# Performance work log

Hardware: AMD Instinct MI355X
Metric: run time of the kernel (lower is better)

The kernel has to match this reference:

```python
import jax, jax.numpy as jnp
import numpy as np
from jax import lax

B, S, D, H, O = 128, 256, 128, 512, 25
TEMP = 0.1


def _init(key, shape, scale):
    return jax.random.uniform(key, shape, jnp.float32, -scale, scale)


def setup_inputs() -> dict:
    key = jax.random.key(0)
    ks = jax.random.split(key, 24)
    sH = 1.0 / np.sqrt(H)
    s2H = 1.0 / np.sqrt(2 * H)
    sD = 1.0 / np.sqrt(D)
    inp = {
        "x": jax.random.normal(ks[0], (B, S, D), jnp.float32),
        "noise_u": jnp.clip(jax.random.uniform(ks[1], (S, B, 1), jnp.float32), 1e-6, 1 - 1e-6),
        # layer_cin: Linear(D, H)
        "w_cin": _init(ks[2], (D, H), sD), "b_cin": _init(ks[3], (H,), sD),
        # layer_c MLP: 2H->2H (x3, ReLU) -> 1
        "w1": _init(ks[4], (2 * H, 2 * H), s2H), "b1": _init(ks[5], (2 * H,), s2H),
        "w2": _init(ks[6], (2 * H, 2 * H), s2H), "b2": _init(ks[7], (2 * H,), s2H),
        "w3": _init(ks[8], (2 * H, 2 * H), s2H), "b3": _init(ks[9], (2 * H,), s2H),
        "w4": _init(ks[10], (2 * H, 1), s2H), "b4": _init(ks[11], (1,), s2H),
        # GRUCell(H, H): gates ordered (r, z, n)
        "w_ih": _init(ks[12], (H, 3 * H), sH), "b_ih": _init(ks[13], (3 * H,), sH),
        "w_hh": _init(ks[14], (H, 3 * H), sH), "b_hh": _init(ks[15], (3 * H,), sH),
        # output Linear(H, O)
        "w_out": _init(ks[16], (H, O), sH), "b_out": _init(ks[17], (O,), sH),
    }
    return inp


def _gru_cell(x, h, w_ih, b_ih, w_hh, b_hh):
    gx = x @ w_ih + b_ih  # [B, 3H]
    gh = h @ w_hh + b_hh
    xr, xz, xn = jnp.split(gx, 3, axis=-1)
    hr, hz, hn = jnp.split(gh, 3, axis=-1)
    r = jax.nn.sigmoid(xr + hr)
    z = jax.nn.sigmoid(xz + hz)
    n = jnp.tanh(xn + r * hn)
    return (1.0 - z) * n + z * h


def reference(x, noise_u, w_cin, b_cin, w1, b1, w2, b2, w3, b3, w4, b4,
              w_ih, b_ih, w_hh, b_hh, w_out, b_out):
    xs = jnp.transpose(x, (1, 0, 2))  # [S, B, D]

    def step(carry, inp):
        c, h, n = carry
        x_t, u = inp
        c_in = jnp.tanh(x_t @ w_cin + b_cin)  # [B, H]
        com = jnp.concatenate([c, c_in], axis=1)  # [B, 2H]
        z = jax.nn.relu(com @ w1 + b1)
        z = jax.nn.relu(z @ w2 + b2)
        z = jax.nn.relu(z @ w3 + b3)
        alpha_logit = z @ w4 + b4  # [B, 1]
        # RelaxedBernoulli(temp=0.1).sample(): sigmoid((logits + logistic noise)/T), detached
        logistic = jnp.log(u) - jnp.log1p(-u)
        alpha = lax.stop_gradient(jax.nn.sigmoid((alpha_logit + logistic) / TEMP))
        h_gru = _gru_cell(c, h, w_ih, b_ih, w_hh, b_hh)
        h_new = h * (1.0 - alpha) + alpha * h_gru
        new_n = n * (1.0 - alpha) + 1.0
        c_new = (c * n * (1.0 - alpha) + c_in) / new_n
        return (c_new, h_new, new_n), None

    c0 = jnp.zeros((B, H), x.dtype)
    h0 = jnp.zeros((B, H), x.dtype)
    n0 = jnp.zeros((B, 1), x.dtype)
    (c, h, n), _ = lax.scan(step, (c0, h0, n0), (xs, noise_u))
    h = _gru_cell(c, h, w_ih, b_ih, w_hh, b_hh)  # final post-loop GRU step
    return h @ w_out + b_out
```

## Files before the change

kernel.cpp:

```cpp
#include <hip/hip_runtime.h>
#include <math.h>

#define SLEN 256
#define BSZ  128
#define DIN  128
#define HSZ  512
#define HH2  1024
#define GG3  1536
#define OSZ  25

typedef _Float16 h8 __attribute__((ext_vector_type(8)));
typedef float    f4 __attribute__((ext_vector_type(4)));

struct P_t {
  const float *x, *noise, *b_cin, *b1, *b2, *b3, *w4, *b4, *b_ih, *b_hh, *w_out, *b_out;
  _Float16 *WT1, *WT2, *WT3, *WTih, *WThh, *WTcin;
  _Float16 *FW1, *FW2, *FW3, *FWih, *FWhh;
  _Float16 *CIN, *COMlo, *Z1, *Z2, *HF16;
  float *LOGI, *GX, *GH, *PART, *HF32, *CF32, *NF32;
  float *out;
};

__device__ __forceinline__ f4 mfma16(h8 a, h8 b, f4 c) {
  return __builtin_amdgcn_mfma_f32_16x16x32_f16(a, b, c, 0, 0, 0);
}

__global__ __launch_bounds__(256) void transpose_cvt(const float* __restrict__ src,
    _Float16* __restrict__ dst, int K, int N) {
  __shared__ float tl[32][33];
  int nt = N >> 5;
  int bx = blockIdx.x % nt, by = blockIdx.x / nt;
  int n0 = bx << 5, k0 = by << 5;
  int tx = threadIdx.x & 31, ty = threadIdx.x >> 5;
#pragma unroll
  for (int i = 0; i < 4; ++i) {
    int r = ty + (i << 3);
    tl[r][tx] = src[(size_t)(k0 + r) * N + n0 + tx];
  }
  __syncthreads();
#pragma unroll
  for (int i = 0; i < 4; ++i) {
    int r = ty + (i << 3);
    dst[(size_t)(n0 + r) * K + k0 + tx] = (_Float16)tl[tx][r];
  }
}

__global__ __launch_bounds__(512) void fragpack(const _Float16* __restrict__ src,
    _Float16* __restrict__ dst, int K) {
  int ct = blockIdx.x;
  int chunks = (K / 32) * 64;
  for (int idx = threadIdx.x; idx < chunks; idx += 512) {
    int i = idx >> 6, lane = idx & 63;
    int mlw = lane & 15, qw = lane >> 4;
    *(h8*)(dst + ((size_t)ct * (K / 32) + i) * 512 + (size_t)lane * 8) =
        *(const h8*)(src + ((size_t)ct * 16 + mlw) * K + i * 32 + qw * 8);
  }
}

__global__ __launch_bounds__(256) void cin_kernel(P_t P) {
  int tid = blockIdx.x * blockDim.x + threadIdx.x;
  if (tid < SLEN * BSZ) {
    float u = P.noise[tid];
    P.LOGI[tid] = logf(u) - log1pf(-u);
  }
  int gw = tid >> 6, lane = tid & 63;
  int nw = (gridDim.x * blockDim.x) >> 6;
  int ml = lane & 15, q = lane >> 4;
  const int MT = (SLEN * BSZ) / 16;
  for (int tt = gw; tt < MT * 8; tt += nw) {
    int mt = tt & (MT - 1), nt = tt / MT;
    int m0 = mt * 16, n0 = nt * 64;
    int m = m0 + ml, b = m & 127, s = m >> 7;
    const float* ap = P.x + ((size_t)b * SLEN + s) * DIN + q * 8;
    const _Float16* bp = P.WTcin + (size_t)(n0 + ml) * DIN + q * 8;
    f4 a0 = {0,0,0,0}, a1 = a0, a2 = a0, a3 = a0;
#pragma unroll
    for (int k = 0; k < DIN; k += 32) {
      f4 lo = *(const f4*)(ap + k);
      f4 hi = *(const f4*)(ap + k + 4);
      h8 av;
      av[0] = (_Float16)lo[0]; av[1] = (_Float16)lo[1];
      av[2] = (_Float16)lo[2]; av[3] = (_Float16)lo[3];
      av[4] = (_Float16)hi[0]; av[5] = (_Float16)hi[1];
      av[6] = (_Float16)hi[2]; av[7] = (_Float16)hi[3];
      a0 = mfma16(av, *(const h8*)(bp + k),            a0);
      a1 = mfma16(av, *(const h8*)(bp + 16*DIN + k),   a1);
      a2 = mfma16(av, *(const h8*)(bp + 32*DIN + k),   a2);
      a3 = mfma16(av, *(const h8*)(bp + 48*DIN + k),   a3);
    }
#pragma unroll
    for (int r = 0; r < 4; ++r) {
      int row = m0 + q * 4 + r;
      int c0 = n0 + ml;
      P.CIN[(size_t)row * HSZ + c0     ] = (_Float16)tanhf(a0[r] + P.b_cin[c0]);
      P.CIN[(size_t)row * HSZ + c0 + 16] = (_Float16)tanhf(a1[r] + P.b_cin[c0 + 16]);
      P.CIN[(size_t)row * HSZ + c0 + 32] = (_Float16)tanhf(a2[r] + P.b_cin[c0 + 32]);
      P.CIN[(size_t)row * HSZ + c0 + 48] = (_Float16)tanhf(a3[r] + P.b_cin[c0 + 48]);
    }
  }
}

__global__ __launch_bounds__(256) void init_kernel(P_t P) {
  int idx = blockIdx.x * 256 + threadIdx.x;
  if (idx < BSZ * HSZ) {
    P.HF32[idx] = 0.f; P.CF32[idx] = 0.f;
    P.HF16[idx] = (_Float16)0.f; P.COMlo[idx] = (_Float16)0.f;
  }
  if (idx < BSZ) P.NF32[idx] = 0.f;
}

__global__ __launch_bounds__(256) void step_a(P_t P, int t, int base) {
  const int tid = threadIdx.x;
  const int lane = tid & 63, wv = tid >> 6;
  const int ml = lane & 15, q = lane >> 4;
  const int g = base + blockIdx.x * 4 + wv;
  f4 acc = {0.f, 0.f, 0.f, 0.f};
  if (g < 512) {
    int rt = g & 7, ct = g >> 3;
    int m0 = rt * 16, col = ct * 16 + ml;
    const _Float16* a0 = P.COMlo + (size_t)(m0 + ml) * HSZ + q * 8;
    const _Float16* a1 = P.CIN + ((size_t)t * BSZ + m0 + ml) * HSZ + q * 8;
    const _Float16* bp = P.FW1 + (size_t)ct * 32 * 512 + (size_t)lane * 8;
#pragma unroll
    for (int i = 0; i < 16; ++i)
      acc = mfma16(*(const h8*)(a0 + i * 32), *(const h8*)(bp + (size_t)i * 512), acc);
#pragma unroll
    for (int i = 0; i < 16; ++i)
      acc = mfma16(*(const h8*)(a1 + i * 32), *(const h8*)(bp + (size_t)(16 + i) * 512), acc);
    float bia = P.b1[col];
#pragma unroll
    for (int j = 0; j < 4; ++j)
      P.Z1[(size_t)(m0 + q * 4 + j) * HH2 + col] = (_Float16)fmaxf(acc[j] + bia, 0.f);
  } else if (g < 1280) {
    int u = g - 512, rt = u & 7, ct = u >> 3;
    int m0 = rt * 16, col = ct * 16 + ml;
    const _Float16* a0 = P.COMlo + (size_t)(m0 + ml) * HSZ + q * 8;
    const _Float16* bp = P.FWih + (size_t)ct * 16 * 512 + (size_t)lane * 8;
#pragma unroll
    for (int i = 0; i < 16; ++i)
      acc = mfma16(*(const h8*)(a0 + i * 32), *(const h8*)(bp + (size_t)i * 512), acc);
    float bia = P.b_ih[col];
#pragma unroll
    for (int j = 0; j < 4; ++j)
      P.GX[(size_t)(m0 + q * 4 + j) * GG3 + col] = acc[j] + bia;
  } else {
    int u = g - 1280, rt = u & 7, ct = u >> 3;
    int m0 = rt * 16, col = ct * 16 + ml;
    const _Float16* a0 = P.HF16 + (size_t)(m0 + ml) * HSZ + q * 8;
    const _Float16* bp = P.FWhh + (size_t)ct * 16 * 512 + (size_t)lane * 8;
#pragma unroll
    for (int i = 0; i < 16; ++i)
      acc = mfma16(*(const h8*)(a0 + i * 32), *(const h8*)(bp + (size_t)i * 512), acc);
    float bia = P.b_hh[col];
#pragma unroll
    for (int j = 0; j < 4; ++j)
      P.GH[(size_t)(m0 + q * 4 + j) * GG3 + col] = acc[j] + bia;
  }
}

__global__ __launch_bounds__(256) void step_b(P_t P) {
  const int tid = threadIdx.x;
  const int lane = tid & 63, wv = tid >> 6;
  const int ml = lane & 15, q = lane >> 4;
  const int g = blockIdx.x * 4 + wv;
  int rt = g & 7, ct = g >> 3;
  int m0 = rt * 16, col = ct * 16 + ml;
  const _Float16* a0 = P.Z1 + (size_t)(m0 + ml) * HH2 + q * 8;
  const _Float16* bp = P.FW2 + (size_t)ct * 32 * 512 + (size_t)lane * 8;
  f4 acc = {0.f, 0.f, 0.f, 0.f};
#pragma unroll
  for (int i = 0; i < 32; ++i)
    acc = mfma16(*(const h8*)(a0 + i * 32), *(const h8*)(bp + (size_t)i * 512), acc);
  float bia = P.b2[col];
#pragma unroll
  for (int j = 0; j < 4; ++j)
    P.Z2[(size_t)(m0 + q * 4 + j) * HH2 + col] = (_Float16)fmaxf(acc[j] + bia, 0.f);
}

__global__ __launch_bounds__(256) void step_c(P_t P) {
  const int tid = threadIdx.x;
  const int lane = tid & 63, wv = tid >> 6;
  const int ml = lane & 15, q = lane >> 4;
  const int g = blockIdx.x * 4 + wv;
  int rt = g & 7, ct = g >> 3;
  int m0 = rt * 16, col = ct * 16 + ml;
  const _Float16* a0 = P.Z2 + (size_t)(m0 + ml) * HH2 + q * 8;
  const _Float16* bp = P.FW3 + (size_t)ct * 32 * 512 + (size_t)lane * 8;
  f4 acc = {0.f, 0.f, 0.f, 0.f};
#pragma unroll
  for (int i = 0; i < 32; ++i)
    acc = mfma16(*(const h8*)(a0 + i * 32), *(const h8*)(bp + (size_t)i * 512), acc);
  float bia = P.b3[col], w4v = P.w4[col];
#pragma unroll
  for (int j = 0; j < 4; ++j) {
    float v = fmaxf(acc[j] + bia, 0.f) * w4v;
    v += __shfl_xor(v, 1); v += __shfl_xor(v, 2);
    v += __shfl_xor(v, 4); v += __shfl_xor(v, 8);
    if (ml == 0) P.PART[(size_t)ct * BSZ + m0 + q * 4 + j] = v;
  }
}

__global__ __launch_bounds__(512) void step_d(P_t P, int t) {
  __shared__ float sa[4];
  const int r = blockIdx.x, tid = threadIdx.x;
  if (tid < 64) {
    float v = P.PART[(size_t)tid * BSZ + r];
#pragma unroll
    for (int off = 32; off > 0; off >>= 1) v += __shfl_xor(v, off);
    if (tid == 0) {
      float lg = (v + P.b4[0] + P.LOGI[(size_t)t * BSZ + r]) * 10.0f;
      float alpha = 1.f / (1.f + expf(-lg));
      float om = 1.f - alpha;
      float n_old = P.NF32[r];
      float nnew = n_old * om + 1.f;
      P.NF32[r] = nnew;
      sa[0] = alpha; sa[1] = om; sa[2] = n_old * om; sa[3] = nnew;
    }
  }
  __syncthreads();
  float alpha = sa[0], om = sa[1], nom = sa[2], nnew = sa[3];
  int col = tid;
  size_t go = (size_t)r * GG3 + col;
  float xr = P.GX[go], xz = P.GX[go + 512], xn = P.GX[go + 1024];
  float hr = P.GH[go], hz = P.GH[go + 512], hn = P.GH[go + 1024];
  float rg = 1.f / (1.f + expf(-(xr + hr)));
  float zg = 1.f / (1.f + expf(-(xz + hz)));
  float ng = tanhf(xn + rg * hn);
  size_t ho = (size_t)r * HSZ + col;
  float h_old = P.HF32[ho];
  float hg = (1.f - zg) * ng + zg * h_old;
  float hnew = h_old * om + alpha * hg;
  P.HF32[ho] = hnew; P.HF16[ho] = (_Float16)hnew;
  float c_old = P.CF32[ho];
  float cin_t = (float)P.CIN[((size_t)t * BSZ + r) * HSZ + col];
  float cnew = (c_old * nom + cin_t) / nnew;
  P.CF32[ho] = cnew; P.COMlo[ho] = (_Float16)cnew;
}

__global__ __launch_bounds__(512) void final_kernel(P_t P) {
  __shared__ float hf[512];
  const int r = blockIdx.x, tid = threadIdx.x;
  const int lane = tid & 63, wv = tid >> 6;
  {
    int col = tid;
    size_t go = (size_t)r * GG3 + col;
    float xr = P.GX[go], xz = P.GX[go + 512], xn = P.GX[go + 1024];
    float hr = P.GH[go], hz = P.GH[go + 512], hn = P.GH[go + 1024];
    float rg = 1.f / (1.f + expf(-(xr + hr)));
    float zg = 1.f / (1.f + expf(-(xz + hz)));
    float ng = tanhf(xn + rg * hn);
    float h_old = P.HF32[(size_t)r * HSZ + col];
    hf[col] = (1.f - zg) * ng + zg * h_old;
  }
  __syncthreads();
  for (int c = wv; c < OSZ; c += 8) {
    float v = 0.f;
#pragma unroll
    for (int j = 0; j < 8; ++j)
      v += hf[lane + 64 * j] * P.w_out[(size_t)(lane + 64 * j) * OSZ + c];
#pragma unroll
    for (int off = 32; off > 0; off >>= 1) v += __shfl_xor(v, off);
    if (lane == 0) P.out[r * OSZ + c] = v + P.b_out[c];
  }
}

extern "C" void kernel_launch(void* const* d_in, const int* in_sizes, int n_in,
                              void* d_out, int out_size, void* d_ws, size_t ws_size,
                              hipStream_t stream) {
  const float* x     = (const float*)d_in[0];
  const float* noise = (const float*)d_in[1];
  const float* w_cin = (const float*)d_in[2];
  const float* b_cin = (const float*)d_in[3];
  const float* w1    = (const float*)d_in[4];
  const float* b1    = (const float*)d_in[5];
  const float* w2    = (const float*)d_in[6];
  const float* b2    = (const float*)d_in[7];
  const float* w3    = (const float*)d_in[8];
  const float* b3    = (const float*)d_in[9];
  const float* w4    = (const float*)d_in[10];
  const float* b4    = (const float*)d_in[11];
  const float* w_ih  = (const float*)d_in[12];
  const float* b_ih  = (const float*)d_in[13];
  const float* w_hh  = (const float*)d_in[14];
  const float* b_hh  = (const float*)d_in[15];
  const float* w_out = (const float*)d_in[16];
  const float* b_out = (const float*)d_in[17];

  char* ws = (char*)d_ws;
  size_t off = 0;
  auto alloc = [&](size_t bytes) -> void* {
    void* p = ws + off;
    off = (off + bytes + 255) & ~(size_t)255;
    return p;
  };

  P_t P;
  P.x = x; P.noise = noise; P.b_cin = b_cin; P.b1 = b1; P.b2 = b2; P.b3 = b3;
  P.w4 = w4; P.b4 = b4; P.b_ih = b_ih; P.b_hh = b_hh; P.w_out = w_out; P.b_out = b_out;
  P.WT1   = (_Float16*)alloc((size_t)HH2 * HH2 * 2);
  P.WT2   = (_Float16*)alloc((size_t)HH2 * HH2 * 2);
  P.WT3   = (_Float16*)alloc((size_t)HH2 * HH2 * 2);
  P.WTih  = (_Float16*)alloc((size_t)GG3 * HSZ * 2);
  P.WThh  = (_Float16*)alloc((size_t)GG3 * HSZ * 2);
  P.WTcin = (_Float16*)alloc((size_t)HSZ * DIN * 2);
  P.FW1   = (_Float16*)alloc((size_t)HH2 * HH2 * 2);
  P.FW2   = (_Float16*)alloc((size_t)HH2 * HH2 * 2);
  P.FW3   = (_Float16*)alloc((size_t)HH2 * HH2 * 2);
  P.FWih  = (_Float16*)alloc((size_t)GG3 * HSZ * 2);
  P.FWhh  = (_Float16*)alloc((size_t)GG3 * HSZ * 2);
  P.CIN   = (_Float16*)alloc((size_t)SLEN * BSZ * HSZ * 2);
  P.COMlo = (_Float16*)alloc((size_t)BSZ * HSZ * 2);
  P.Z1    = (_Float16*)alloc((size_t)BSZ * HH2 * 2);
  P.Z2    = (_Float16*)alloc((size_t)BSZ * HH2 * 2);
  P.HF16  = (_Float16*)alloc((size_t)BSZ * HSZ * 2);
  P.LOGI  = (float*)alloc((size_t)SLEN * BSZ * 4);
  P.GX    = (float*)alloc((size_t)BSZ * GG3 * 4);
  P.GH    = (float*)alloc((size_t)BSZ * GG3 * 4);
  P.PART  = (float*)alloc((size_t)64 * BSZ * 4);
  P.HF32  = (float*)alloc((size_t)BSZ * HSZ * 4);
  P.CF32  = (float*)alloc((size_t)BSZ * HSZ * 4);
  P.NF32  = (float*)alloc((size_t)BSZ * 4);
  P.out   = (float*)d_out;

  transpose_cvt<<<(HH2/32)*(HH2/32), 256, 0, stream>>>(w1, P.WT1, HH2, HH2);
  transpose_cvt<<<(HH2/32)*(HH2/32), 256, 0, stream>>>(w2, P.WT2, HH2, HH2);
  transpose_cvt<<<(HH2/32)*(HH2/32), 256, 0, stream>>>(w3, P.WT3, HH2, HH2);
  transpose_cvt<<<(GG3/32)*(HSZ/32), 256, 0, stream>>>(w_ih, P.WTih, HSZ, GG3);
  transpose_cvt<<<(GG3/32)*(HSZ/32), 256, 0, stream>>>(w_hh, P.WThh, HSZ, GG3);
  transpose_cvt<<<(HSZ/32)*(DIN/32), 256, 0, stream>>>(w_cin, P.WTcin, DIN, HSZ);
  fragpack<<<HH2/16, 512, 0, stream>>>(P.WT1, P.FW1, HH2);
  fragpack<<<HH2/16, 512, 0, stream>>>(P.WT2, P.FW2, HH2);
  fragpack<<<HH2/16, 512, 0, stream>>>(P.WT3, P.FW3, HH2);
  fragpack<<<GG3/16, 512, 0, stream>>>(P.WTih, P.FWih, HSZ);
  fragpack<<<GG3/16, 512, 0, stream>>>(P.WThh, P.FWhh, HSZ);

  cin_kernel<<<1024, 256, 0, stream>>>(P);
  init_kernel<<<256, 256, 0, stream>>>(P);

  for (int t = 0; t < SLEN; ++t) {
    step_a<<<512, 256, 0, stream>>>(P, t, 0);
    step_b<<<128, 256, 0, stream>>>(P);
    step_c<<<128, 256, 0, stream>>>(P);
    step_d<<<BSZ, 512, 0, stream>>>(P, t);
  }
  step_a<<<384, 256, 0, stream>>>(P, 0, 512);
  final_kernel<<<BSZ, 512, 0, stream>>>(P);
}
```

Before: 6.966 ms.

## Fuse GRU/state update into next step's GEMM kernel with double-buffered state

This removes the separate per-timestep state-update kernel. Each step_a block now reduces the alpha partials itself, recomputes the c and h updates for its 16-row tile into shared memory as the fp16 GEMM operand, and has one designated block write the fp32 state back. h, c, n, GX and GH are double-buffered by timestep parity so reads and writes don't race, and the PART layout is transposed for vectorized reduction. The aim is to cut one kernel launch and a global round-trip per step. In exchange, GX/GH reads and the sigmoid/tanh work are done redundantly across many blocks.

```diff
diff --git a/kernel.cpp b/kernel.cpp
--- a/kernel.cpp
+++ b/kernel.cpp
@@ -16,7 +16,7 @@
   const float *x, *noise, *b_cin, *b1, *b2, *b3, *w4, *b4, *b_ih, *b_hh, *w_out, *b_out;
   _Float16 *WT1, *WT2, *WT3, *WTih, *WThh, *WTcin;
   _Float16 *FW1, *FW2, *FW3, *FWih, *FWhh;
-  _Float16 *CIN, *COMlo, *Z1, *Z2, *HF16;
+  _Float16 *CIN, *Z1, *Z2;
   float *LOGI, *GX, *GH, *PART, *HF32, *CF32, *NF32;
   float *out;
 };
@@ -24,6 +24,7 @@
 __device__ __forceinline__ f4 mfma16(h8 a, h8 b, f4 c) {
   return __builtin_amdgcn_mfma_f32_16x16x32_f16(a, b, c, 0, 0, 0);
 }
+__device__ __forceinline__ float sigmf(float x) { return 1.f / (1.f + expf(-x)); }
 
 __global__ __launch_bounds__(256) void transpose_cvt(const float* __restrict__ src,
     _Float16* __restrict__ dst, int K, int N) {
@@ -103,58 +104,135 @@
 __global__ __launch_bounds__(256) void init_kernel(P_t P) {
   int idx = blockIdx.x * 256 + threadIdx.x;
   if (idx < BSZ * HSZ) {
-    P.HF32[idx] = 0.f; P.CF32[idx] = 0.f;
-    P.HF16[idx] = (_Float16)0.f; P.COMlo[idx] = (_Float16)0.f;
-  }
-  if (idx < BSZ) P.NF32[idx] = 0.f;
-}
-
-__global__ __launch_bounds__(256) void step_a(P_t P, int t, int base) {
-  const int tid = threadIdx.x;
-  const int lane = tid & 63, wv = tid >> 6;
+    P.HF32[idx] = 0.f; P.HF32[idx + BSZ * HSZ] = 0.f;
+    P.CF32[idx] = 0.f; P.CF32[idx + BSZ * HSZ] = 0.f;
+  }
+  if (idx < 2 * BSZ) P.NF32[idx] = 0.f;
+}
+
+__global__ __launch_bounds__(256) void step_a(P_t P, int t, int tail) {
+  __shared__ __align__(16) _Float16 sA[8192];
+  __shared__ float s_al[16], s_om[16], s_nom[16], s_nnew[16];
+  const int tid = threadIdx.x, lane = tid & 63, wv = tid >> 6;
   const int ml = lane & 15, q = lane >> 4;
-  const int g = base + blockIdx.x * 4 + wv;
+  const int b = blockIdx.x + (tail ? 128 : 0);
+  int role, rt, cg;
+  if (b < 128)      { role = 0; rt = b >> 4; cg = b & 15; }
+  else if (b < 320) { int u = b - 128; role = 1; rt = u / 24; cg = u - rt * 24; }
+  else              { int u = b - 320; role = 2; rt = u / 24; cg = u - rt * 24; }
+  const int m0 = rt * 16;
+  const int pm1 = (t + 1) & 1;
+  const int pm2 = t & 1;
+
+  if (t > 0) {
+    if (wv == 0) {
+      const float* pp = P.PART + (size_t)(m0 + ml) * 64 + q * 16;
+      f4 p0 = *(const f4*)pp, p1 = *(const f4*)(pp + 4),
+         p2 = *(const f4*)(pp + 8), p3 = *(const f4*)(pp + 12);
+      float s = p0[0]+p0[1]+p0[2]+p0[3] + p1[0]+p1[1]+p1[2]+p1[3]
+              + p2[0]+p2[1]+p2[2]+p2[3] + p3[0]+p3[1]+p3[2]+p3[3];
+      s += __shfl_xor(s, 16); s += __shfl_xor(s, 32);
+      float lg = (s + P.b4[0] + P.LOGI[(size_t)(t - 1) * BSZ + m0 + ml]) * 10.0f;
+      float al = sigmf(lg), om = 1.f - al;
+      if (q == 0) {
+        float n_old = P.NF32[pm2 * BSZ + m0 + ml];
+        float nom = n_old * om, nnew = nom + 1.f;
+        s_al[ml] = al; s_om[ml] = om; s_nom[ml] = nom; s_nnew[ml] = nnew;
+        if (role == 0 && cg == 0) P.NF32[pm1 * BSZ + m0 + ml] = nnew;
+      }
+    }
+    __syncthreads();
+    if (role <= 1) {
+      float nom = s_nom[ml], rnn = 1.f / s_nnew[ml];
+      const float*    cf = P.CF32 + ((size_t)pm2 * BSZ + m0 + ml) * HSZ;
+      const _Float16* ci = P.CIN + ((size_t)(t - 1) * BSZ + m0 + ml) * HSZ;
+      float* cw = (role == 0 && cg == 0)
+                  ? (P.CF32 + ((size_t)pm1 * BSZ + m0 + ml) * HSZ) : nullptr;
+#pragma unroll
+      for (int ic = 0; ic < 4; ++ic) {
+        int i = wv * 4 + ic, colb = i * 32 + q * 8;
+        f4 c0 = *(const f4*)(cf + colb), c1 = *(const f4*)(cf + colb + 4);
+        h8 cin8 = *(const h8*)(ci + colb);
+        h8 hv; f4 o0, o1;
+#pragma unroll
+        for (int j = 0; j < 4; ++j) {
+          o0[j] = (c0[j] * nom + (float)cin8[j])     * rnn;
+          o1[j] = (c1[j] * nom + (float)cin8[4 + j]) * rnn;
+          hv[j] = (_Float16)o0[j]; hv[4 + j] = (_Float16)o1[j];
+        }
+        *(h8*)(sA + i * 512 + lane * 8) = hv;
+        if (cw) { *(f4*)(cw + colb) = o0; *(f4*)(cw + colb + 4) = o1; }
+      }
+    } else {
+      float al = s_al[ml], om = s_om[ml];
+      const float* gx = P.GX + (size_t)pm1 * BSZ * GG3 + (size_t)(m0 + ml) * GG3;
+      const float* gh = P.GH + (size_t)pm1 * BSZ * GG3 + (size_t)(m0 + ml) * GG3;
+      const float* hf = P.HF32 + ((size_t)pm2 * BSZ + m0 + ml) * HSZ;
+      float* hw = (cg == 0) ? (P.HF32 + ((size_t)pm1 * BSZ + m0 + ml) * HSZ) : nullptr;
+#pragma unroll
+      for (int ic = 0; ic < 4; ++ic) {
+        int i = wv * 4 + ic, colb = i * 32 + q * 8;
+        f4 xr0 = *(const f4*)(gx + colb),        xr1 = *(const f4*)(gx + colb + 4);
+        f4 xz0 = *(const f4*)(gx + colb + 512),  xz1 = *(const f4*)(gx + colb + 516);
+        f4 xn0 = *(const f4*)(gx + colb + 1024), xn1 = *(const f4*)(gx + colb + 1028);
+        f4 hr0 = *(const f4*)(gh + colb),        hr1 = *(const f4*)(gh + colb + 4);
+        f4 hz0 = *(const f4*)(gh + colb + 512),  hz1 = *(const f4*)(gh + colb + 516);
+        f4 hn0 = *(const f4*)(gh + colb + 1024), hn1 = *(const f4*)(gh + colb + 1028);
+        f4 h0 = *(const f4*)(hf + colb), h1 = *(const f4*)(hf + colb + 4);
+        h8 hv; f4 o0, o1;
+#pragma unroll
+        for (int j = 0; j < 4; ++j) {
+          float rg = sigmf(xr0[j] + hr0[j]);
+          float zg = sigmf(xz0[j] + hz0[j]);
+          float ng = tanhf(xn0[j] + rg * hn0[j]);
+          o0[j] = h0[j] * om + al * ((1.f - zg) * ng + zg * h0[j]);
+          rg = sigmf(xr1[j] + hr1[j]);
+          zg = sigmf(xz1[j] + hz1[j]);
+          ng = tanhf(xn1[j] + rg * hn1[j]);
+          o1[j] = h1[j] * om + al * ((1.f - zg) * ng + zg * h1[j]);
+          hv[j] = (_Float16)o0[j]; hv[4 + j] = (_Float16)o1[j];
+        }
+        *(h8*)(sA + i * 512 + lane * 8) = hv;
+        if (hw) { *(f4*)(hw + colb) = o0; *(f4*)(hw + colb + 4) = o1; }
+      }
+    }
+  } else {
+    h8 z;
+#pragma unroll
+    for (int j = 0; j < 8; ++j) z[j] = (_Float16)0.f;
+    for (int idx = tid; idx < 1024; idx += 256) *(h8*)(sA + idx * 8) = z;
+  }
+  __syncthreads();
+
+  const int ct = cg * 4 + wv;
   f4 acc = {0.f, 0.f, 0.f, 0.f};
-  if (g < 512) {
-    int rt = g & 7, ct = g >> 3;
-    int m0 = rt * 16, col = ct * 16 + ml;
-    const _Float16* a0 = P.COMlo + (size_t)(m0 + ml) * HSZ + q * 8;
-    const _Float16* a1 = P.CIN + ((size_t)t * BSZ + m0 + ml) * HSZ + q * 8;
-    const _Float16* bp = P.FW1 + (size_t)ct * 32 * 512 + (size_t)lane * 8;
+  if (role == 0) {
+    const _Float16* bp = P.FW1 + (size_t)ct * 32 * 512 + lane * 8;
+    const _Float16* sa = sA + lane * 8;
+    const _Float16* ci = P.CIN + ((size_t)t * BSZ + m0 + ml) * HSZ + q * 8;
 #pragma unroll
     for (int i = 0; i < 16; ++i)
-      acc = mfma16(*(const h8*)(a0 + i * 32), *(const h8*)(bp + (size_t)i * 512), acc);
+      acc = mfma16(*(const h8*)(sa + i * 512), *(const h8*)(bp + (size_t)i * 512), acc);
 #pragma unroll
     for (int i = 0; i < 16; ++i)
-      acc = mfma16(*(const h8*)(a1 + i * 32), *(const h8*)(bp + (size_t)(16 + i) * 512), acc);
+      acc = mfma16(*(const h8*)(ci + i * 32), *(const h8*)(bp + (size_t)(16 + i) * 512), acc);
+    int col = ct * 16 + ml;
     float bia = P.b1[col];
 #pragma unroll
     for (int j = 0; j < 4; ++j)
       P.Z1[(size_t)(m0 + q * 4 + j) * HH2 + col] = (_Float16)fmaxf(acc[j] + bia, 0.f);
-  } else if (g < 1280) {
-    int u = g - 512, rt = u & 7, ct = u >> 3;
-    int m0 = rt * 16, col = ct * 16 + ml;
-    const _Float16* a0 = P.COMlo + (size_t)(m0 + ml) * HSZ + q * 8;
-    const _Float16* bp = P.FWih + (size_t)ct * 16 * 512 + (size_t)lane * 8;
+  } else {
+    const _Float16* bp = ((role == 1) ? P.FWih : P.FWhh) + (size_t)ct * 16 * 512 + lane * 8;
+    const _Float16* sa = sA + lane * 8;
 #pragma unroll
     for (int i = 0; i < 16; ++i)
-      acc = mfma16(*(const h8*)(a0 + i * 32), *(const h8*)(bp + (size_t)i * 512), acc);
-    float bia = P.b_ih[col];
+      acc = mfma16(*(const h8*)(sa + i * 512), *(const h8*)(bp + (size_t)i * 512), acc);
+    int col = ct * 16 + ml;
+    float bia = (role == 1) ? P.b_ih[col] : P.b_hh[col];
+    float* gd = ((role == 1) ? P.GX : P.GH) + (size_t)pm2 * BSZ * GG3;
 #pragma unroll
     for (int j = 0; j < 4; ++j)
-      P.GX[(size_t)(m0 + q * 4 + j) * GG3 + col] = acc[j] + bia;
-  } else {
-    int u = g - 1280, rt = u & 7, ct = u >> 3;
-    int m0 = rt * 16, col = ct * 16 + ml;
-    const _Float16* a0 = P.HF16 + (size_t)(m0 + ml) * HSZ + q * 8;
-    const _Float16* bp = P.FWhh + (size_t)ct * 16 * 512 + (size_t)lane * 8;
-#pragma unroll
-    for (int i = 0; i < 16; ++i)
-      acc = mfma16(*(const h8*)(a0 + i * 32), *(const h8*)(bp + (size_t)i * 512), acc);
-    float bia = P.b_hh[col];
-#pragma unroll
-    for (int j = 0; j < 4; ++j)
-      P.GH[(size_t)(m0 + q * 4 + j) * GG3 + col] = acc[j] + bia;
+      gd[(size_t)(m0 + q * 4 + j) * GG3 + col] = acc[j] + bia;
   }
 }
 
@@ -196,45 +274,8 @@
     float v = fmaxf(acc[j] + bia, 0.f) * w4v;
     v += __shfl_xor(v, 1); v += __shfl_xor(v, 2);
     v += __shfl_xor(v, 4); v += __shfl_xor(v, 8);
-    if (ml == 0) P.PART[(size_t)ct * BSZ + m0 + q * 4 + j] = v;
-  }
-}
-
-__global__ __launch_bounds__(512) void step_d(P_t P, int t) {
-  __shared__ float sa[4];
-  const int r = blockIdx.x, tid = threadIdx.x;
-  if (tid < 64) {
-    float v = P.PART[(size_t)tid * BSZ + r];
-#pragma unroll
-    for (int off = 32; off > 0; off >>= 1) v += __shfl_xor(v, off);
-    if (tid == 0) {
-      float lg = (v + P.b4[0] + P.LOGI[(size_t)t * BSZ + r]) * 10.0f;
-      float alpha = 1.f / (1.f + expf(-lg));
-      float om = 1.f - alpha;
-      float n_old = P.NF32[r];
-      float nnew = n_old * om + 1.f;
-      P.NF32[r] = nnew;
-      sa[0] = alpha; sa[1] = om; sa[2] = n_old * om; sa[3] = nnew;
-    }
-  }
-  __syncthreads();
-  float alpha = sa[0], om = sa[1], nom = sa[2], nnew = sa[3];
-  int col = tid;
-  size_t go = (size_t)r * GG3 + col;
-  float xr = P.GX[go], xz = P.GX[go + 512], xn = P.GX[go + 1024];
-  float hr = P.GH[go], hz = P.GH[go + 512], hn = P.GH[go + 1024];
-  float rg = 1.f / (1.f + expf(-(xr + hr)));
-  float zg = 1.f / (1.f + expf(-(xz + hz)));
-  float ng = tanhf(xn + rg * hn);
-  size_t ho = (size_t)r * HSZ + col;
-  float h_old = P.HF32[ho];
-  float hg = (1.f - zg) * ng + zg * h_old;
-  float hnew = h_old * om + alpha * hg;
-  P.HF32[ho] = hnew; P.HF16[ho] = (_Float16)hnew;
-  float c_old = P.CF32[ho];
-  float cin_t = (float)P.CIN[((size_t)t * BSZ + r) * HSZ + col];
-  float cnew = (c_old * nom + cin_t) / nnew;
-  P.CF32[ho] = cnew; P.COMlo[ho] = (_Float16)cnew;
+    if (ml == 0) P.PART[(size_t)(m0 + q * 4 + j) * 64 + ct] = v;
+  }
 }
 
 __global__ __launch_bounds__(512) void final_kernel(P_t P) {
@@ -246,10 +287,10 @@
     size_t go = (size_t)r * GG3 + col;
     float xr = P.GX[go], xz = P.GX[go + 512], xn = P.GX[go + 1024];
     float hr = P.GH[go], hz = P.GH[go + 512], hn = P.GH[go + 1024];
-    float rg = 1.f / (1.f + expf(-(xr + hr)));
-    float zg = 1.f / (1.f + expf(-(xz + hz)));
+    float rg = sigmf(xr + hr);
+    float zg = sigmf(xz + hz);
     float ng = tanhf(xn + rg * hn);
-    float h_old = P.HF32[(size_t)r * HSZ + col];
+    float h_old = P.HF32[(size_t)BSZ * HSZ + (size_t)r * HSZ + col];
     hf[col] = (1.f - zg) * ng + zg * h_old;
   }
   __syncthreads();
@@ -309,17 +350,15 @@
   P.FWih  = (_Float16*)alloc((size_t)GG3 * HSZ * 2);
   P.FWhh  = (_Float16*)alloc((size_t)GG3 * HSZ * 2);
   P.CIN   = (_Float16*)alloc((size_t)SLEN * BSZ * HSZ * 2);
-  P.COMlo = (_Float16*)alloc((size_t)BSZ * HSZ * 2);
   P.Z1    = (_Float16*)alloc((size_t)BSZ * HH2 * 2);
   P.Z2    = (_Float16*)alloc((size_t)BSZ * HH2 * 2);
-  P.HF16  = (_Float16*)alloc((size_t)BSZ * HSZ * 2);
   P.LOGI  = (float*)alloc((size_t)SLEN * BSZ * 4);
-  P.GX    = (float*)alloc((size_t)BSZ * GG3 * 4);
-  P.GH    = (float*)alloc((size_t)BSZ * GG3 * 4);
-  P.PART  = (float*)alloc((size_t)64 * BSZ * 4);
-  P.HF32  = (float*)alloc((size_t)BSZ * HSZ * 4);
-  P.CF32  = (float*)alloc((size_t)BSZ * HSZ * 4);
-  P.NF32  = (float*)alloc((size_t)BSZ * 4);
+  P.GX    = (float*)alloc((size_t)2 * BSZ * GG3 * 4);
+  P.GH    = (float*)alloc((size_t)2 * BSZ * GG3 * 4);
+  P.PART  = (float*)alloc((size_t)BSZ * 64 * 4);
+  P.HF32  = (float*)alloc((size_t)2 * BSZ * HSZ * 4);
+  P.CF32  = (float*)alloc((size_t)2 * BSZ * HSZ * 4);
+  P.NF32  = (float*)alloc((size_t)2 * BSZ * 4);
   P.out   = (float*)d_out;
 
   transpose_cvt<<<(HH2/32)*(HH2/32), 256, 0, stream>>>(w1, P.WT1, HH2, HH2);
@@ -341,8 +380,7 @@
     step_a<<<512, 256, 0, stream>>>(P, t, 0);
     step_b<<<128, 256, 0, stream>>>(P);
     step_c<<<128, 256, 0, stream>>>(P);
-    step_d<<<BSZ, 512, 0, stream>>>(P, t);
-  }
-  step_a<<<384, 256, 0, stream>>>(P, 0, 512);
+  }
+  step_a<<<384, 256, 0, stream>>>(P, SLEN, 1);
   final_kernel<<<BSZ, 512, 0, stream>>>(P);
 }
```

Result: slower. 8.086 ms (+16.1%).
